# Kernel optimization log

Measured on AMD Instinct MI355X. Metric: run time of the kernel, lower is better.

The kernel has to match this reference:

```python
import jax, jax.numpy as jnp
import numpy as np

ALPHA = 0.2  # LeakyReLU negative slope
EDGE_NUM = 3


def _gat(q_nodes, v, adj, a_q, a_v):
    # q_nodes: (b,n,d_hidden), v: (b,n,d_model), adj: (b,n,n)
    # e_ij = LeakyReLU(a_q . h_i + a_v . v_j)  (decomposition of a^T[h_i;v_j])
    s_q = jnp.einsum('bnd,d->bn', q_nodes, a_q)
    s_v = jnp.einsum('bne,e->bn', v, a_v)
    e = jax.nn.leaky_relu(s_q[:, :, None] + s_v[:, None, :], negative_slope=ALPHA)
    e = jnp.where(adj > 0, e, -1e9)
    attn = jax.nn.softmax(e, axis=-1)           # (b,n,n)
    return jnp.einsum('bij,bje->bie', attn, v)  # (b,n,d_model)


def setup_inputs() -> dict:
    key = jax.random.key(0)
    ks = jax.random.split(key, 16)
    b, n, dh, dm = 8, 1024, 512, 512
    s = 0.02
    inp = {
        'nodes': jax.random.normal(ks[0], (b, n, dh), dtype=jnp.float32),
        'mask': jax.random.randint(ks[1], (2, b, n, n), 0, 2, dtype=jnp.int32),
        'node_type': jax.random.randint(ks[2], (b, n), 0, 5, dtype=jnp.int64),
        # edge-typed linears (bias=False), stacked over 3 edge types
        'W_in': jax.random.normal(ks[3], (EDGE_NUM, dh, dm), dtype=jnp.float32) * s,
        'W_out': jax.random.normal(ks[4], (EDGE_NUM, dh, dm), dtype=jnp.float32) * s,
        # GAT attention vectors, split into query / value halves
        'a_in_q': jax.random.normal(ks[5], (dh,), dtype=jnp.float32) * s,
        'a_in_v': jax.random.normal(ks[6], (dm,), dtype=jnp.float32) * s,
        'a_out_q': jax.random.normal(ks[7], (dh,), dtype=jnp.float32) * s,
        'a_out_v': jax.random.normal(ks[8], (dm,), dtype=jnp.float32) * s,
        # GGNN propagator (reset / update / transform)
        'W_r': jax.random.normal(ks[9], (3 * dm, dm), dtype=jnp.float32) * s,
        'b_r': jnp.zeros((dm,), dtype=jnp.float32),
        'W_z': jax.random.normal(ks[10], (3 * dm, dm), dtype=jnp.float32) * s,
        'b_z': jnp.zeros((dm,), dtype=jnp.float32),
        'W_t': jax.random.normal(ks[11], (3 * dm, dm), dtype=jnp.float32) * s,
        'b_t': jnp.zeros((dm,), dtype=jnp.float32),
    }
    return inp


def reference(nodes, mask, node_type, W_in, W_out, a_in_q, a_in_v, a_out_q, a_out_v,
              W_r, b_r, W_z, b_z, W_t, b_t):
    # type masks for tags 2,3,4 -> (3,b,n)
    tags = jnp.arange(2, 2 + EDGE_NUM, dtype=node_type.dtype)
    tmask = (node_type[None, :, :] == tags[:, None, None]).astype(nodes.dtype)
    # edge-typed linear + masked sum over edge types
    node_in = jnp.sum(jnp.einsum('bnd,tde->tbne', nodes, W_in) * tmask[..., None], axis=0)
    node_out = jnp.sum(jnp.einsum('bnd,tde->tbne', nodes, W_out) * tmask[..., None], axis=0)
    # GAT-style masked attention (in / out edges); dropout = identity (eval)
    h_in = _gat(nodes, node_in, mask[0], a_in_q, a_in_v)
    h_out = _gat(nodes, node_out, mask[1], a_out_q, a_out_v)
    # GGNN gated propagator
    a = jnp.concatenate([h_in, h_out, nodes], axis=-1)
    r = jax.nn.sigmoid(a @ W_r + b_r)
    z = jax.nn.sigmoid(a @ W_z + b_z)
    joint = jnp.concatenate([h_in, h_out, r * nodes], axis=-1)
    h_hat = jnp.tanh(joint @ W_t + b_t)
    return (1.0 - z) * nodes + z * h_hat
```

## Files before the change

kernel.cpp:

```cpp
#include <hip/hip_runtime.h>
#include <hip/hip_bf16.h>
#include <stdint.h>

typedef unsigned short u16;
typedef __attribute__((ext_vector_type(8))) short bf16x8;
typedef __attribute__((ext_vector_type(4))) float floatx4;

__device__ __forceinline__ float bf2f(u16 v){ return __uint_as_float(((unsigned)v)<<16); }
__device__ __forceinline__ u16 f2bf(float f){
  unsigned u = __float_as_uint(f);
  unsigned r = 0x7fffu + ((u>>16)&1u);
  return (u16)((u+r)>>16);
}
__device__ __forceinline__ float lrelu(float x){ return x > 0.f ? x : 0.2f*x; }
__device__ __forceinline__ float sigm(float t){
  t = fminf(fmaxf(t, -30.f), 30.f);
  return 1.f/(1.f + __expf(-t));
}

#define GLOAD16(ldsdst, gsrc) \
  __builtin_amdgcn_global_load_lds((const __attribute__((address_space(1))) void*)(gsrc), \
      (__attribute__((address_space(3))) void*)(ldsdst), 16, 0, 0)

__global__ void k_detect(const u16* __restrict__ nodes_raw,
                         const int* __restrict__ ntype_raw, int* flags)
{
  __shared__ int s_wild, s_nz;
  if (threadIdx.x == 0){ s_wild = 0; s_nz = 0; }
  __syncthreads();
  int wild = 0;
#pragma unroll
  for (int i = 0; i < 16; i++){
    u16 w = nodes_raw[threadIdx.x*16 + i];
    int e = (w >> 7) & 0xFF;
    if (e != 0 && (e < 102 || e > 152)) wild++;
  }
  int nz = 0;
  if (threadIdx.x < 255 && ntype_raw[2*threadIdx.x + 1] != 0) nz = 1;
  atomicAdd(&s_wild, wild);
  atomicAdd(&s_nz, nz);
  __syncthreads();
  if (threadIdx.x == 0){
    flags[0] = (s_wild > 1024) ? 1 : 0;
    flags[1] = (s_nz == 0) ? 1 : 0;
  }
}

struct CanonDesc {
  const void* src[13];
  u16*        dst[13];
  int startBlk[13];
  int n4[13];
};
__global__ __launch_bounds__(256)
void k_canon_all(CanonDesc d, u16* __restrict__ X, const int* __restrict__ flags)
{
  int blk = blockIdx.x;
  int seg = 0;
#pragma unroll
  for (int s = 1; s < 13; s++) if (blk >= d.startBlk[s]) seg = s;
  int i = (blk - d.startBlk[seg])*256 + threadIdx.x;
  if (i >= d.n4[seg]) return;
  uint2 bits;
  if (flags[0]) {
    float4 v = ((const float4*)d.src[seg])[i];
    ushort4 o2;
    o2.x = f2bf(v.x); o2.y = f2bf(v.y); o2.z = f2bf(v.z); o2.w = f2bf(v.w);
    bits = *(uint2*)&o2;
  } else {
    bits = ((const uint2*)d.src[seg])[i];
  }
  ((uint2*)d.dst[seg])[i] = bits;
  if (seg == 0) {
    int e0 = i*4;
    long r = e0 >> 9;
    int  c = e0 & 511;
    *(uint2*)&X[r*2048 + c] = bits;
  }
}

__global__ void k_build_idx(const int* __restrict__ ntype, const int* __restrict__ flags,
                            int* __restrict__ idx, int* __restrict__ cnt)
{
  __shared__ int c[3];
  if (threadIdx.x < 3) c[threadIdx.x] = 0;
  __syncthreads();
  const int i64 = flags[1];
  for (int i = threadIdx.x; i < 8192; i += 256){
    int t = i64 ? ntype[2*i] : ntype[i];
    if (t >= 2 && t <= 4){
      int p = atomicAdd(&c[t-2], 1);
      idx[(t-2)*8192 + p] = i;
    }
  }
  __syncthreads();
  if (threadIdx.x < 3) cnt[threadIdx.x] = c[threadIdx.x];
}

template<int MODE, class Epi>
__global__ __launch_bounds__(256)
void gemm_bt(const u16* __restrict__ A, int ldA, long sAz,
             const u16* __restrict__ B, int ldB, long sBz,
             int K, Epi epi)
{
  __shared__ __align__(16) u16 As[2][128][64];
  __shared__ __align__(16) u16 Bs[2][128][64];
  int bm, bn, bz;
  if (MODE == 0){ bm = blockIdx.x; bn = blockIdx.y; bz = blockIdx.z; }
  else          { bz = blockIdx.x; bn = blockIdx.y; bm = blockIdx.z; }
  const int tid  = threadIdx.x;
  const int lane = tid & 63;
  const int wave = tid >> 6;
  const int wm = (wave & 1) << 6;
  const int wn = (wave >> 1) << 6;
  const int mrow = lane & 15;
  const int quad = lane >> 4;

  const u16* Ab = A + (long)bz*sAz + (long)bm*128*ldA;
  const u16* Bb = B + (long)bz*sBz + (long)bn*128*ldB;
  const int srow = tid >> 3;
  const int scol = (tid & 7) << 3;
  const u16* gA[4];
  const u16* gB[4];
#pragma unroll
  for (int i=0;i<4;i++){
    gA[i] = Ab + (long)(srow + 32*i)*ldA + scol;
    gB[i] = Bb + (long)(srow + 32*i)*ldB + scol;
  }

  floatx4 acc[4][4];
#pragma unroll
  for (int i=0;i<4;i++)
#pragma unroll
    for (int j=0;j<4;j++) acc[i][j] = 0.f;

  auto issue = [&](int buf){
#pragma unroll
    for (int i=0;i<4;i++){ GLOAD16(&As[buf][srow+32*i][scol], gA[i]); gA[i] += 64; }
#pragma unroll
    for (int i=0;i<4;i++){ GLOAD16(&Bs[buf][srow+32*i][scol], gB[i]); gB[i] += 64; }
  };

  issue(0);
  const int nIter = K >> 6;
  for (int it = 0; it < nIter; ++it) {
    const int cur = it & 1;
    asm volatile("s_waitcnt vmcnt(0)" ::: "memory");
    __syncthreads();
    if (it + 1 < nIter) issue(cur ^ 1);
#pragma unroll
    for (int k32 = 0; k32 < 2; ++k32) {
      bf16x8 af[4], bfr[4];
#pragma unroll
      for (int i=0;i<4;i++) af[i]  = *(const bf16x8*)&As[cur][wm + i*16 + mrow][k32*32 + quad*8];
#pragma unroll
      for (int i=0;i<4;i++) bfr[i] = *(const bf16x8*)&Bs[cur][wn + i*16 + mrow][k32*32 + quad*8];
#pragma unroll
      for (int mi=0;mi<4;mi++)
#pragma unroll
        for (int ni=0;ni<4;ni++)
          acc[mi][ni] = __builtin_amdgcn_mfma_f32_16x16x32_bf16(af[mi], bfr[ni], acc[mi][ni], 0,0,0);
    }
  }

#pragma unroll
  for (int mi=0;mi<4;mi++)
#pragma unroll
    for (int ni=0;ni<4;ni++) {
      const int col  = (bn<<7) + wn + ni*16 + mrow;
      const int row0 = (bm<<7) + wm + mi*16 + quad*4;
#pragma unroll
      for (int r=0;r<4;r++)
        epi(row0 + r, col, bz, acc[mi][ni][r]);
    }
}

__global__ __launch_bounds__(256)
void gemm_typed(const u16* __restrict__ A, const u16* __restrict__ B,
                const int* __restrict__ idx, const int* __restrict__ cnt,
                u16* __restrict__ node_in, u16* __restrict__ node_out)
{
  const int bz = blockIdx.z;
  const int count = cnt[bz];
  const int m0 = blockIdx.x << 7;
  if (m0 >= count) return;
  __shared__ __align__(16) u16 As[2][128][64];
  __shared__ __align__(16) u16 Bs[2][128][64];
  const int bn = blockIdx.y;
  const int tid  = threadIdx.x;
  const int lane = tid & 63;
  const int wave = tid >> 6;
  const int wm = (wave & 1) << 6;
  const int wn = (wave >> 1) << 6;
  const int mrow = lane & 15;
  const int quad = lane >> 4;
  const int srow = tid >> 3;
  const int scol = (tid & 7) << 3;
  const int* myidx = idx + bz*8192;

  const u16* gA[4];
  const u16* gB[4];
#pragma unroll
  for (int i=0;i<4;i++){
    int r = m0 + srow + 32*i;
    if (r >= count) r = count - 1;
    gA[i] = A + (long)myidx[r]*512 + scol;
    gB[i] = B + (long)bz*1024*512 + (long)(bn*128 + srow + 32*i)*512 + scol;
  }

  floatx4 acc[4][4];
#pragma unroll
  for (int i=0;i<4;i++)
#pragma unroll
    for (int j=0;j<4;j++) acc[i][j] = 0.f;

  auto issue = [&](int buf){
#pragma unroll
    for (int i=0;i<4;i++){ GLOAD16(&As[buf][srow+32*i][scol], gA[i]); gA[i] += 64; }
#pragma unroll
    for (int i=0;i<4;i++){ GLOAD16(&Bs[buf][srow+32*i][scol], gB[i]); gB[i] += 64; }
  };

  issue(0);
  for (int it = 0; it < 8; ++it) {
    const int cur = it & 1;
    asm volatile("s_waitcnt vmcnt(0)" ::: "memory");
    __syncthreads();
    if (it + 1 < 8) issue(cur ^ 1);
#pragma unroll
    for (int k32 = 0; k32 < 2; ++k32) {
      bf16x8 af[4], bfr[4];
#pragma unroll
      for (int i=0;i<4;i++) af[i]  = *(const bf16x8*)&As[cur][wm + i*16 + mrow][k32*32 + quad*8];
#pragma unroll
      for (int i=0;i<4;i++) bfr[i] = *(const bf16x8*)&Bs[cur][wn + i*16 + mrow][k32*32 + quad*8];
#pragma unroll
      for (int mi=0;mi<4;mi++)
#pragma unroll
        for (int ni=0;ni<4;ni++)
          acc[mi][ni] = __builtin_amdgcn_mfma_f32_16x16x32_bf16(af[mi], bfr[ni], acc[mi][ni], 0,0,0);
    }
  }

#pragma unroll
  for (int mi=0;mi<4;mi++) {
    const int lr0 = wm + mi*16 + quad*4;
#pragma unroll
    for (int r=0;r<4;r++) {
      const int lr = lr0 + r;
      if (m0 + lr >= count) continue;
      const long orig = myidx[m0 + lr];
#pragma unroll
      for (int ni=0;ni<4;ni++) {
        const int col = (bn<<7) + wn + ni*16 + mrow;
        u16 h = f2bf(acc[mi][ni][r]);
        if (col < 512) node_in [orig*512 + col]       = h;
        else           node_out[orig*512 + (col-512)] = h;
      }
    }
  }
}

struct EpiPV {
  const float* il; u16* X;
  __device__ void operator()(int row, int col, int bz, float v) const {
    long gr = (long)(bz & 7)*1024 + row;
    int colOff = 512 + ((bz >> 3) << 9);
    X[gr*2048 + colOff + col] = f2bf(v * il[(long)(bz>>3)*8192 + gr]);
  }
};
struct EpiG1 {
  const u16* nodes; const u16* b_r; const u16* b_z; u16* X; u16* zbuf;
  __device__ void operator()(int row, int col, int bz, float v) const {
    if (col < 512) {
      float r = sigm(v + bf2f(b_r[col]));
      X[(long)row*2048 + 1536 + col] = f2bf(r * bf2f(nodes[(long)row*512 + col]));
    } else {
      int c = col - 512;
      zbuf[(long)row*512 + c] = f2bf(sigm(v + bf2f(b_z[c])));
    }
  }
};
struct EpiG2 {
  const u16* zbuf; const u16* nodes; const u16* b_t; const int* flags; void* out;
  __device__ void operator()(int row, int col, int bz, float v) const {
    long idx = (long)row*512 + col;
    float t = fminf(fmaxf(v + bf2f(b_t[col]), -15.f), 15.f);
    float h = 2.f*sigm(2.f*t) - 1.f;
    float z = bf2f(zbuf[idx]);
    float nv = bf2f(nodes[idx]);
    float o2 = (1.f - z)*nv + z*h;
    if (flags[0]) ((float*)out)[idx] = o2;
    else          ((u16*)out)[idx]   = f2bf(o2);
  }
};

struct TrDesc {
  const u16* src[9]; u16* dst[9]; int rot[9]; int ldD[9]; int rows[9]; int modK[9];
};
__global__ __launch_bounds__(256)
void k_wtrans(TrDesc d)
{
  __shared__ u16 tile[32][33];
  const int z = blockIdx.z;
  const int r0 = blockIdx.y*32;
  if (r0 >= d.rows[z]) return;
  const u16* src = d.src[z];
  u16* dst = d.dst[z];
  const int c0 = blockIdx.x*32;
  const int tx = threadIdx.x, ty = threadIdx.y;
#pragma unroll
  for (int i=0;i<32;i+=8)
    tile[ty+i][tx] = src[(long)(r0+ty+i)*512 + c0 + tx];
  __syncthreads();
  const int k0 = (r0 + d.rot[z]) % d.modK[z];
#pragma unroll
  for (int i=0;i<32;i+=8)
    dst[(long)(c0+ty+i)*d.ldD[z] + k0 + tx] = tile[tx][ty+i];
}

__global__ __launch_bounds__(256)
void k_vtrans(const u16* __restrict__ nin, const u16* __restrict__ nout,
              u16* __restrict__ vin, u16* __restrict__ vout)
{
  __shared__ u16 tile[32][33];
  const int z = blockIdx.z;
  const int b = z & 7;
  const u16* src = (z < 8 ? nin : nout) + (long)b*1024*512;
  u16* dst = (z < 8 ? vin : vout) + (long)b*512*1024;
  const int c0 = blockIdx.x*32, r0 = blockIdx.y*32;
  const int tx = threadIdx.x, ty = threadIdx.y;
#pragma unroll
  for (int i=0;i<32;i+=8)
    tile[ty+i][tx] = src[(long)(r0+ty+i)*512 + c0 + tx];
  __syncthreads();
#pragma unroll
  for (int i=0;i<32;i+=8)
    dst[(long)(c0+ty+i)*1024 + r0 + tx] = tile[tx][ty+i];
}

__device__ __forceinline__ void load8f(float* f, const u16* p){
  uint4 q = *(const uint4*)p;
  unsigned w[4] = {q.x, q.y, q.z, q.w};
#pragma unroll
  for (int i=0;i<4;i++){ f[2*i] = bf2f((u16)(w[i]&0xffffu)); f[2*i+1] = bf2f((u16)(w[i]>>16)); }
}

__global__ __launch_bounds__(256)
void k_svec(const u16* __restrict__ nodes, const u16* __restrict__ nin, const u16* __restrict__ nout,
            const u16* __restrict__ aiq, const u16* __restrict__ aiv,
            const u16* __restrict__ aoq, const u16* __restrict__ aov,
            float* sq_all, float* sv_all)
{
  const int lane = threadIdx.x & 63, wave = threadIdx.x >> 6;
  const long row = (long)blockIdx.x*4 + wave;
  const int c = lane << 3;
  float xn[8], xi[8], xo[8], q1[8], v1[8], q2[8], v2[8];
  load8f(xn, nodes + row*512 + c);
  load8f(xi, nin   + row*512 + c);
  load8f(xo, nout  + row*512 + c);
  load8f(q1, aiq + c); load8f(v1, aiv + c);
  load8f(q2, aoq + c); load8f(v2, aov + c);
  float s0=0,s1=0,s2=0,s3=0;
#pragma unroll
  for (int j=0;j<8;j++){ s0 += xn[j]*q1[j]; s1 += xn[j]*q2[j]; s2 += xi[j]*v1[j]; s3 += xo[j]*v2[j]; }
#pragma unroll
  for (int off=32; off; off>>=1){
    s0 += __shfl_xor(s0, off);
    s1 += __shfl_xor(s1, off);
    s2 += __shfl_xor(s2, off);
    s3 += __shfl_xor(s3, off);
  }
  if (lane==0){
    sq_all[row] = s0; sq_all[8192 + row] = s1;
    sv_all[row] = s2; sv_all[8192 + row] = s3;
  }
}

__global__ __launch_bounds__(256)
void k_stats(const int* __restrict__ mask, const float* __restrict__ sq_all,
             const float* __restrict__ sv_all, u16* __restrict__ P, float* __restrict__ il_all)
{
  const int lane = threadIdx.x & 63, wave = threadIdx.x >> 6;
  const long row = (long)blockIdx.x*4 + wave;
  const long gr  = (long)blockIdx.y*8192 + row;
  const int* mrow = mask + gr*1024;
  const float* svb = sv_all + (long)blockIdx.y*8192 + (row >> 10)*1024;
  const float qs = sq_all[gr];
  float m = -3.0e38f;
  float e[4][4];
#pragma unroll
  for (int it=0; it<4; ++it) {
    int j = it*256 + lane*4;
    int4 mk = *(const int4*)&mrow[j];
    float4 s = *(const float4*)&svb[j];
    e[it][0] = mk.x > 0 ? lrelu(qs + s.x) : -1e9f;
    e[it][1] = mk.y > 0 ? lrelu(qs + s.y) : -1e9f;
    e[it][2] = mk.z > 0 ? lrelu(qs + s.z) : -1e9f;
    e[it][3] = mk.w > 0 ? lrelu(qs + s.w) : -1e9f;
    m = fmaxf(m, fmaxf(fmaxf(e[it][0], e[it][1]), fmaxf(e[it][2], e[it][3])));
  }
#pragma unroll
  for (int off=32; off; off>>=1) m = fmaxf(m, __shfl_xor(m, off));
  float l = 0.f;
#pragma unroll
  for (int it=0; it<4; ++it) {
    int j = it*256 + lane*4;
    float p0 = __expf(e[it][0] - m), p1 = __expf(e[it][1] - m);
    float p2 = __expf(e[it][2] - m), p3 = __expf(e[it][3] - m);
    ushort4 pk;
    pk.x = f2bf(p0); pk.y = f2bf(p1); pk.z = f2bf(p2); pk.w = f2bf(p3);
    *(ushort4*)&P[gr*1024 + j] = pk;
    l += (p0 + p1) + (p2 + p3);
  }
#pragma unroll
  for (int off=32; off; off>>=1) l += __shfl_xor(l, off);
  if (lane==0) il_all[gr] = 1.f / l;
}

extern "C" void kernel_launch(void* const* d_in, const int* in_sizes, int n_in,
                              void* d_out, int out_size, void* d_ws, size_t ws_size,
                              hipStream_t stream)
{
  const void* nodes_r = d_in[0];
  const int*  mask    = (const int*)d_in[1];
  const int*  ntype   = (const int*)d_in[2];

  char* base = (char*)d_ws;
  size_t o = 0;
  auto alloc = [&](size_t bytes){ void* p = base + o; o += (bytes + 255) & ~size_t(255); return p; };
  int*  flags   = (int*)alloc(256);
  int*  cnt     = (int*)alloc(256);
  int*  idx     = (int*)alloc(3ll*8192*4);
  u16* cn_nodes = (u16*)alloc(8192ll*512*2);
  u16* cn_Win   = (u16*)alloc(3ll*512*512*2);
  u16* cn_Wout  = (u16*)alloc(3ll*512*512*2);
  u16* cn_Wr    = (u16*)alloc(1536ll*512*2);
  u16* cn_Wz    = (u16*)alloc(1536ll*512*2);
  u16* cn_Wt    = (u16*)alloc(1536ll*512*2);
  u16* cn_aiq   = (u16*)alloc(512*2);
  u16* cn_aiv   = (u16*)alloc(512*2);
  u16* cn_aoq   = (u16*)alloc(512*2);
  u16* cn_aov   = (u16*)alloc(512*2);
  u16* cn_br    = (u16*)alloc(512*2);
  u16* cn_bz    = (u16*)alloc(512*2);
  u16* cn_bt    = (u16*)alloc(512*2);
  u16* node_in  = (u16*)alloc(8192ll*512*2);
  u16* node_out = (u16*)alloc(8192ll*512*2);
  u16* Vt       = (u16*)alloc(16ll*512*1024*2);
  u16* X        = (u16*)alloc(8192ll*2048*2);
  u16* P        = (u16*)alloc(16ll*1024*1024*2);
  u16* Wio_t    = (u16*)alloc(3ll*1024*512*2);
  u16* Wrz_t    = (u16*)alloc(1024ll*1536*2);
  u16* Wt_t     = (u16*)alloc(512ll*1536*2);
  float* sq_all = (float*)alloc(16384*4);
  float* sv_all = (float*)alloc(16384*4);
  float* il_all = (float*)alloc(16384*4);
  u16* zbuf = node_in;

  hipMemsetAsync(node_in, 0, 2ll*8192*512*2, stream);

  k_detect<<<1, 256, 0, stream>>>((const u16*)nodes_r, ntype, flags);

  CanonDesc cd;
  const int canonN[13] = {8192*512, 3*512*512, 3*512*512, 1536*512, 1536*512, 1536*512,
                          512,512,512,512,512,512,512};
  u16* canonDst[13] = {cn_nodes, cn_Win, cn_Wout, cn_Wr, cn_Wz, cn_Wt,
                       cn_aiq, cn_aiv, cn_aoq, cn_aov, cn_br, cn_bz, cn_bt};
  const int canonSrcIdx[13] = {0,3,4,9,11,13,5,6,7,8,10,12,14};
  int blk = 0;
  for (int s=0;s<13;s++){
    cd.src[s] = d_in[canonSrcIdx[s]];
    cd.dst[s] = canonDst[s];
    cd.n4[s]  = canonN[s]/4;
    cd.startBlk[s] = blk;
    blk += (cd.n4[s] + 255)/256;
  }
  k_canon_all<<<blk, 256, 0, stream>>>(cd, X, flags);

  k_build_idx<<<1, 256, 0, stream>>>(ntype, flags, idx, cnt);

  TrDesc td;
  td.src[0]=cn_Wr; td.src[1]=cn_Wz; td.src[2]=cn_Wt;
  td.dst[0]=Wrz_t; td.dst[1]=Wrz_t + 512ll*1536; td.dst[2]=Wt_t;
  td.rot[0]=512; td.rot[1]=512; td.rot[2]=0;
  td.ldD[0]=1536; td.ldD[1]=1536; td.ldD[2]=1536;
  td.rows[0]=1536; td.rows[1]=1536; td.rows[2]=1536;
  td.modK[0]=1536; td.modK[1]=1536; td.modK[2]=1536;
  for (int t=0;t<3;t++){
    td.src[3+t]=cn_Win  + (long)t*512*512; td.dst[3+t]=Wio_t + (long)t*1024*512;
    td.src[6+t]=cn_Wout + (long)t*512*512; td.dst[6+t]=Wio_t + (long)t*1024*512 + 512ll*512;
    td.rot[3+t]=td.rot[6+t]=0; td.ldD[3+t]=td.ldD[6+t]=512;
    td.rows[3+t]=td.rows[6+t]=512; td.modK[3+t]=td.modK[6+t]=512;
  }
  k_wtrans<<<dim3(16,48,9), dim3(32,8), 0, stream>>>(td);

  gemm_typed<<<dim3(64,8,3), 256, 0, stream>>>(cn_nodes, Wio_t, idx, cnt, node_in, node_out);

  k_vtrans<<<dim3(16,32,16), dim3(32,8), 0, stream>>>(node_in, node_out, Vt, Vt + 8ll*512*1024);

  k_svec<<<2048, 256, 0, stream>>>(cn_nodes, node_in, node_out, cn_aiq, cn_aiv, cn_aoq, cn_aov,
                                   sq_all, sv_all);

  k_stats<<<dim3(2048,2), 256, 0, stream>>>(mask, sq_all, sv_all, P, il_all);

  gemm_bt<1><<<dim3(16,4,8), 256, 0, stream>>>(P, 1024, 1024ll*1024, Vt, 1024, 512ll*1024, 1024,
                                               EpiPV{il_all, X});

  gemm_bt<0><<<dim3(64,8,1), 256, 0, stream>>>(X, 2048, 0ll, Wrz_t, 1536, 0ll, 1536,
                                               EpiG1{cn_nodes, cn_br, cn_bz, X, zbuf});
  gemm_bt<0><<<dim3(64,4,1), 256, 0, stream>>>(X + 512, 2048, 0ll, Wt_t, 1536, 0ll, 1536,
                                               EpiG2{zbuf, cn_nodes, cn_bt, flags, (void*)d_out});
}
```

Measured before the change: 379.3 us.

## Swizzle LDS tiles, halve K-step to 32, use 64-wide N tiles for final GEMM

Shared-memory tiles in the GEMM kernels now hold 32-wide K slices, with an XOR swizzle on 16-byte chunks so MFMA fragment reads avoid bank conflicts. LDS usage per block is halved, which may allow more resident blocks. The cost is twice as many loop iterations and barriers. The gemm_bt kernel is templated on N-tile width, and the final transform GEMM uses 64-column tiles on a doubled grid to get more blocks for its small N.

```diff
diff --git a/kernel.cpp b/kernel.cpp
--- a/kernel.cpp
+++ b/kernel.cpp
@@ -21,6 +21,8 @@
 #define GLOAD16(ldsdst, gsrc) \
   __builtin_amdgcn_global_load_lds((const __attribute__((address_space(1))) void*)(gsrc), \
       (__attribute__((address_space(3))) void*)(ldsdst), 16, 0, 0)
+
+__device__ __forceinline__ int swz(int r, int q){ return r*4 + (q ^ ((r>>1)&3)); }
 
 __global__ void k_detect(const u16* __restrict__ nodes_raw,
                          const int* __restrict__ ntype_raw, int* flags)
@@ -97,14 +99,16 @@
   if (threadIdx.x < 3) cnt[threadIdx.x] = c[threadIdx.x];
 }
 
-template<int MODE, class Epi>
+template<int MODE, int NBI, class Epi>
 __global__ __launch_bounds__(256)
 void gemm_bt(const u16* __restrict__ A, int ldA, long sAz,
              const u16* __restrict__ B, int ldB, long sBz,
              int K, Epi epi)
 {
-  __shared__ __align__(16) u16 As[2][128][64];
-  __shared__ __align__(16) u16 Bs[2][128][64];
+  constexpr int BN = NBI*64;
+  constexpr int NT = BN/32;
+  __shared__ __align__(16) u16 As[2][128*32];
+  __shared__ __align__(16) u16 Bs[2][BN*32];
   int bm, bn, bz;
   if (MODE == 0){ bm = blockIdx.x; bn = blockIdx.y; bz = blockIdx.z; }
   else          { bz = blockIdx.x; bn = blockIdx.y; bm = blockIdx.z; }
@@ -112,62 +116,63 @@
   const int lane = tid & 63;
   const int wave = tid >> 6;
   const int wm = (wave & 1) << 6;
-  const int wn = (wave >> 1) << 6;
+  const int wn = (wave >> 1) * (BN/2);
   const int mrow = lane & 15;
   const int quad = lane >> 4;
 
   const u16* Ab = A + (long)bz*sAz + (long)bm*128*ldA;
-  const u16* Bb = B + (long)bz*sBz + (long)bn*128*ldB;
-  const int srow = tid >> 3;
-  const int scol = (tid & 7) << 3;
-  const u16* gA[4];
-  const u16* gB[4];
-#pragma unroll
-  for (int i=0;i<4;i++){
-    gA[i] = Ab + (long)(srow + 32*i)*ldA + scol;
-    gB[i] = Bb + (long)(srow + 32*i)*ldB + scol;
-  }
-
-  floatx4 acc[4][4];
+  const u16* Bb = B + (long)bz*sBz + (long)bn*BN*ldB;
+
+  const int oA0 = tid, oA1 = 256 + tid;
+  const int rA0 = oA0 >> 2, rA1 = oA1 >> 2;
+  const u16* gA0 = Ab + (long)rA0*ldA + (((oA0&3) ^ ((rA0>>1)&3)) << 3);
+  const u16* gA1 = Ab + (long)rA1*ldA + (((oA1&3) ^ ((rA1>>1)&3)) << 3);
+  const u16* gB0 = Bb + (long)rA0*ldB + (((oA0&3) ^ ((rA0>>1)&3)) << 3);
+  const u16* gB1 = (NBI == 2) ? Bb + (long)rA1*ldB + (((oA1&3) ^ ((rA1>>1)&3)) << 3) : nullptr;
+
+  int offA[4], offB[NT];
+#pragma unroll
+  for (int i=0;i<4;i++){ int r = wm + i*16 + mrow; offA[i] = swz(r, quad)*8; }
+#pragma unroll
+  for (int i=0;i<NT;i++){ int r = wn + i*16 + mrow; offB[i] = swz(r, quad)*8; }
+
+  floatx4 acc[4][NT];
 #pragma unroll
   for (int i=0;i<4;i++)
 #pragma unroll
-    for (int j=0;j<4;j++) acc[i][j] = 0.f;
+    for (int j=0;j<NT;j++) acc[i][j] = 0.f;
 
   auto issue = [&](int buf){
-#pragma unroll
-    for (int i=0;i<4;i++){ GLOAD16(&As[buf][srow+32*i][scol], gA[i]); gA[i] += 64; }
-#pragma unroll
-    for (int i=0;i<4;i++){ GLOAD16(&Bs[buf][srow+32*i][scol], gB[i]); gB[i] += 64; }
+    GLOAD16(&As[buf][oA0*8], gA0); gA0 += 32;
+    GLOAD16(&As[buf][oA1*8], gA1); gA1 += 32;
+    GLOAD16(&Bs[buf][oA0*8], gB0); gB0 += 32;
+    if (NBI == 2){ GLOAD16(&Bs[buf][oA1*8], gB1); gB1 += 32; }
   };
 
   issue(0);
-  const int nIter = K >> 6;
+  const int nIter = K >> 5;
   for (int it = 0; it < nIter; ++it) {
     const int cur = it & 1;
     asm volatile("s_waitcnt vmcnt(0)" ::: "memory");
     __syncthreads();
     if (it + 1 < nIter) issue(cur ^ 1);
-#pragma unroll
-    for (int k32 = 0; k32 < 2; ++k32) {
-      bf16x8 af[4], bfr[4];
-#pragma unroll
-      for (int i=0;i<4;i++) af[i]  = *(const bf16x8*)&As[cur][wm + i*16 + mrow][k32*32 + quad*8];
-#pragma unroll
-      for (int i=0;i<4;i++) bfr[i] = *(const bf16x8*)&Bs[cur][wn + i*16 + mrow][k32*32 + quad*8];
-#pragma unroll
-      for (int mi=0;mi<4;mi++)
-#pragma unroll
-        for (int ni=0;ni<4;ni++)
-          acc[mi][ni] = __builtin_amdgcn_mfma_f32_16x16x32_bf16(af[mi], bfr[ni], acc[mi][ni], 0,0,0);
-    }
+    bf16x8 af[4], bfr[NT];
+#pragma unroll
+    for (int i=0;i<4;i++)  af[i]  = *(const bf16x8*)&As[cur][offA[i]];
+#pragma unroll
+    for (int i=0;i<NT;i++) bfr[i] = *(const bf16x8*)&Bs[cur][offB[i]];
+#pragma unroll
+    for (int mi=0;mi<4;mi++)
+#pragma unroll
+      for (int ni=0;ni<NT;ni++)
+        acc[mi][ni] = __builtin_amdgcn_mfma_f32_16x16x32_bf16(af[mi], bfr[ni], acc[mi][ni], 0,0,0);
   }
 
 #pragma unroll
   for (int mi=0;mi<4;mi++)
 #pragma unroll
-    for (int ni=0;ni<4;ni++) {
-      const int col  = (bn<<7) + wn + ni*16 + mrow;
+    for (int ni=0;ni<NT;ni++) {
+      const int col  = bn*BN + wn + ni*16 + mrow;
       const int row0 = (bm<<7) + wm + mi*16 + quad*4;
 #pragma unroll
       for (int r=0;r<4;r++)
@@ -184,8 +189,8 @@
   const int count = cnt[bz];
   const int m0 = blockIdx.x << 7;
   if (m0 >= count) return;
-  __shared__ __align__(16) u16 As[2][128][64];
-  __shared__ __align__(16) u16 Bs[2][128][64];
+  __shared__ __align__(16) u16 As[2][128*32];
+  __shared__ __align__(16) u16 Bs[2][128*32];
   const int bn = blockIdx.y;
   const int tid  = threadIdx.x;
   const int lane = tid & 63;
@@ -194,19 +199,23 @@
   const int wn = (wave >> 1) << 6;
   const int mrow = lane & 15;
   const int quad = lane >> 4;
-  const int srow = tid >> 3;
-  const int scol = (tid & 7) << 3;
   const int* myidx = idx + bz*8192;
 
-  const u16* gA[4];
-  const u16* gB[4];
-#pragma unroll
-  for (int i=0;i<4;i++){
-    int r = m0 + srow + 32*i;
-    if (r >= count) r = count - 1;
-    gA[i] = A + (long)myidx[r]*512 + scol;
-    gB[i] = B + (long)bz*1024*512 + (long)(bn*128 + srow + 32*i)*512 + scol;
-  }
+  const int oA0 = tid, oA1 = 256 + tid;
+  const int rA0 = oA0 >> 2, rA1 = oA1 >> 2;
+  int gr0 = m0 + rA0; if (gr0 >= count) gr0 = count - 1;
+  int gr1 = m0 + rA1; if (gr1 >= count) gr1 = count - 1;
+  const u16* gA0 = A + (long)myidx[gr0]*512 + (((oA0&3) ^ ((rA0>>1)&3)) << 3);
+  const u16* gA1 = A + (long)myidx[gr1]*512 + (((oA1&3) ^ ((rA1>>1)&3)) << 3);
+  const u16* Bb = B + (long)bz*1024*512 + (long)bn*128*512;
+  const u16* gB0 = Bb + (long)rA0*512 + (((oA0&3) ^ ((rA0>>1)&3)) << 3);
+  const u16* gB1 = Bb + (long)rA1*512 + (((oA1&3) ^ ((rA1>>1)&3)) << 3);
+
+  int offA[4], offB[4];
+#pragma unroll
+  for (int i=0;i<4;i++){ int r = wm + i*16 + mrow; offA[i] = swz(r, quad)*8; }
+#pragma unroll
+  for (int i=0;i<4;i++){ int r = wn + i*16 + mrow; offB[i] = swz(r, quad)*8; }
 
   floatx4 acc[4][4];
 #pragma unroll
@@ -215,31 +224,28 @@
     for (int j=0;j<4;j++) acc[i][j] = 0.f;
 
   auto issue = [&](int buf){
-#pragma unroll
-    for (int i=0;i<4;i++){ GLOAD16(&As[buf][srow+32*i][scol], gA[i]); gA[i] += 64; }
-#pragma unroll
-    for (int i=0;i<4;i++){ GLOAD16(&Bs[buf][srow+32*i][scol], gB[i]); gB[i] += 64; }
+    GLOAD16(&As[buf][oA0*8], gA0); gA0 += 32;
+    GLOAD16(&As[buf][oA1*8], gA1); gA1 += 32;
+    GLOAD16(&Bs[buf][oA0*8], gB0); gB0 += 32;
+    GLOAD16(&Bs[buf][oA1*8], gB1); gB1 += 32;
   };
 
   issue(0);
-  for (int it = 0; it < 8; ++it) {
+  for (int it = 0; it < 16; ++it) {
     const int cur = it & 1;
     asm volatile("s_waitcnt vmcnt(0)" ::: "memory");
     __syncthreads();
-    if (it + 1 < 8) issue(cur ^ 1);
-#pragma unroll
-    for (int k32 = 0; k32 < 2; ++k32) {
-      bf16x8 af[4], bfr[4];
-#pragma unroll
-      for (int i=0;i<4;i++) af[i]  = *(const bf16x8*)&As[cur][wm + i*16 + mrow][k32*32 + quad*8];
-#pragma unroll
-      for (int i=0;i<4;i++) bfr[i] = *(const bf16x8*)&Bs[cur][wn + i*16 + mrow][k32*32 + quad*8];
-#pragma unroll
-      for (int mi=0;mi<4;mi++)
-#pragma unroll
-        for (int ni=0;ni<4;ni++)
-          acc[mi][ni] = __builtin_amdgcn_mfma_f32_16x16x32_bf16(af[mi], bfr[ni], acc[mi][ni], 0,0,0);
-    }
+    if (it + 1 < 16) issue(cur ^ 1);
+    bf16x8 af[4], bfr[4];
+#pragma unroll
+    for (int i=0;i<4;i++) af[i]  = *(const bf16x8*)&As[cur][offA[i]];
+#pragma unroll
+    for (int i=0;i<4;i++) bfr[i] = *(const bf16x8*)&Bs[cur][offB[i]];
+#pragma unroll
+    for (int mi=0;mi<4;mi++)
+#pragma unroll
+      for (int ni=0;ni<4;ni++)
+        acc[mi][ni] = __builtin_amdgcn_mfma_f32_16x16x32_bf16(af[mi], bfr[ni], acc[mi][ni], 0,0,0);
   }
 
 #pragma unroll
@@ -504,11 +510,11 @@
 
   k_stats<<<dim3(2048,2), 256, 0, stream>>>(mask, sq_all, sv_all, P, il_all);
 
-  gemm_bt<1><<<dim3(16,4,8), 256, 0, stream>>>(P, 1024, 1024ll*1024, Vt, 1024, 512ll*1024, 1024,
-                                               EpiPV{il_all, X});
-
-  gemm_bt<0><<<dim3(64,8,1), 256, 0, stream>>>(X, 2048, 0ll, Wrz_t, 1536, 0ll, 1536,
-                                               EpiG1{cn_nodes, cn_br, cn_bz, X, zbuf});
-  gemm_bt<0><<<dim3(64,4,1), 256, 0, stream>>>(X + 512, 2048, 0ll, Wt_t, 1536, 0ll, 1536,
-                                               EpiG2{zbuf, cn_nodes, cn_bt, flags, (void*)d_out});
-}
+  gemm_bt<1,2><<<dim3(16,4,8), 256, 0, stream>>>(P, 1024, 1024ll*1024, Vt, 1024, 512ll*1024, 1024,
+                                                 EpiPV{il_all, X});
+
+  gemm_bt<0,2><<<dim3(64,8,1), 256, 0, stream>>>(X, 2048, 0ll, Wrz_t, 1536, 0ll, 1536,
+                                                 EpiG1{cn_nodes, cn_br, cn_bz, X, zbuf});
+  gemm_bt<0,1><<<dim3(64,8,1), 256, 0, stream>>>(X + 512, 2048, 0ll, Wt_t, 1536, 0ll, 1536,
+                                                 EpiG2{zbuf, cn_nodes, cn_bt, flags, (void*)d_out});
+}
```

Measured after the change: 353.0 us. 1.07x faster.
